# Optimization experiments

Hardware: AMD Instinct MI355X
Metric: run time of the kernel (lower is better)

Reference implementation:

```python
import jax, jax.numpy as jnp
import numpy as np

N, D_IN, D_H, D_ATT, N_CLUSTERS, N_CLASSES = 20000, 1024, 512, 256, 10, 4


def setup_inputs() -> dict:
    key = jax.random.key(0)
    ks = jax.random.split(key, 20)
    s = 0.02
    inp = {
        "x_path": jax.random.normal(ks[0], (N, D_IN), dtype=jnp.float32),
        "cluster_id": jax.random.randint(ks[1], (N,), 0, N_CLUSTERS, dtype=jnp.int64 if jax.config.jax_enable_x64 else jnp.int32),
        # per-cluster expert MLPs (phi_i): 1024->512->512
        "W1": jax.random.normal(ks[2], (N_CLUSTERS, D_IN, D_H), dtype=jnp.float32) * s,
        "b1": jnp.zeros((N_CLUSTERS, D_H), dtype=jnp.float32),
        "W2": jax.random.normal(ks[3], (N_CLUSTERS, D_H, D_H), dtype=jnp.float32) * s,
        "b2": jnp.zeros((N_CLUSTERS, D_H), dtype=jnp.float32),
        # attention_net: fc (512->512) then gated attention (L=512, D=256, 1)
        "Wfc": jax.random.normal(ks[4], (D_H, D_H), dtype=jnp.float32) * s,
        "bfc": jnp.zeros((D_H,), dtype=jnp.float32),
        "Wa": jax.random.normal(ks[5], (D_H, D_ATT), dtype=jnp.float32) * s,
        "ba": jnp.zeros((D_ATT,), dtype=jnp.float32),
        "Wb": jax.random.normal(ks[6], (D_H, D_ATT), dtype=jnp.float32) * s,
        "bb": jnp.zeros((D_ATT,), dtype=jnp.float32),
        "Wc": jax.random.normal(ks[7], (D_ATT, 1), dtype=jnp.float32) * s,
        "bc": jnp.zeros((1,), dtype=jnp.float32),
        # rho: 512->256
        "Wrho": jax.random.normal(ks[8], (D_H, D_ATT), dtype=jnp.float32) * s,
        "brho": jnp.zeros((D_ATT,), dtype=jnp.float32),
        # classifier: 256->4
        "Wcls": jax.random.normal(ks[9], (D_ATT, N_CLASSES), dtype=jnp.float32) * s,
        "bcls": jnp.zeros((N_CLASSES,), dtype=jnp.float32),
    }
    return inp


def reference(x_path, cluster_id, W1, b1, W2, b2, Wfc, bfc, Wa, ba, Wb, bb, Wc, bc, Wrho, brho, Wcls, bcls):
    C = W1.shape[0]
    # dispatch mask [N, C]; per-cluster counts
    onehot = jax.nn.one_hot(cluster_id, C, dtype=x_path.dtype)
    counts = jnp.maximum(onehot.sum(axis=0), 1.0)  # [C]
    # per-cluster expert MLP + masked mean-pool (AdaptiveAvgPool1d(1) over instances)
    pooled = []
    for i in range(C):  # small static loop over experts
        h = jax.nn.relu(x_path @ W1[i] + b1[i])      # [N, 512]
        h = jax.nn.relu(h @ W2[i] + b2[i])           # [N, 512]
        pooled.append((onehot[:, i] @ h) / counts[i])  # masked mean -> [512]
    h_cluster = jnp.stack(pooled, axis=0)            # [C, 512]
    # attention_net: fc then gated attention
    h = jax.nn.relu(h_cluster @ Wfc + bfc)           # [C, 512]
    a = jnp.tanh(h @ Wa + ba)                        # [C, 256]
    b = jax.nn.sigmoid(h @ Wb + bb)                  # [C, 256]
    A = ((a * b) @ Wc + bc).T                        # [1, C]
    A = jax.nn.softmax(A, axis=1)
    h_path = A @ h                                   # [1, 512]
    h_path = jax.nn.relu(h_path @ Wrho + brho).squeeze()  # [256]
    logits = (h_path @ Wcls + bcls)[None, :]         # [1, 4]
    Y_hat = jnp.argmax(logits, axis=1, keepdims=True)
    hazards = jax.nn.sigmoid(logits)
    S = jnp.cumprod(1.0 - hazards, axis=1)
    return hazards, S, Y_hat
```

## Files before the change

### kernel.cpp

```cpp
#include <hip/hip_runtime.h>
#include <hip/hip_bf16.h>
#include <math.h>


#define C_NUM 10
#define D_IN 1024
#define D_H 512
#define D_ATT 256
#define N_CLS 4
#define BM 128
#define BMG 64
#define BN 128
#define BKS 64

typedef __attribute__((ext_vector_type(8))) short short8v;
typedef __attribute__((ext_vector_type(4))) short short4v;
typedef __attribute__((ext_vector_type(4))) float f32x4;

__device__ __forceinline__ short f2bf(float f) {
    __hip_bfloat16 h = __float2bfloat16(f);
    return *reinterpret_cast<short*>(&h);
}

__device__ __forceinline__ void gload_lds16(const void* g, void* l) {
    __builtin_amdgcn_global_load_lds((const __attribute__((address_space(1))) unsigned int*)g,
                                     (__attribute__((address_space(3))) unsigned int*)l,
                                     16, 0, 0);
}

__device__ __forceinline__ int xcd_swizzle(int orig, int nwg) {
    int q = nwg >> 3, r = nwg & 7;
    int xcd = orig & 7, base = orig >> 3;
    return (xcd < r ? xcd * (q + 1) : r * (q + 1) + (xcd - r) * q) + base;
}

__global__ __launch_bounds__(256) void k_hist(const int* __restrict__ cid, int* counts, int n) {
    __shared__ int lc[C_NUM];
    int tid = threadIdx.x;
    if (tid < C_NUM) lc[tid] = 0;
    __syncthreads();
    int i = blockIdx.x * 256 + tid;
    if (i < n) atomicAdd(&lc[cid[i]], 1);
    __syncthreads();
    if (tid < C_NUM && lc[tid] > 0) atomicAdd(&counts[tid], lc[tid]);
}

__global__ __launch_bounds__(256) void k_scatter(const int* __restrict__ cid, int* cursor,
                                                 const int* __restrict__ counts,
                                                 int* bucket, int n) {
    __shared__ int lc[C_NUM];
    __shared__ int basev[C_NUM];
    __shared__ int loff[C_NUM + 1];
    int tid = threadIdx.x;
    if (tid < C_NUM) lc[tid] = 0;
    if (tid == 0) {
        int off = 0;
        for (int c2 = 0; c2 < C_NUM; ++c2) {
            loff[c2] = off;
            off += ((counts[c2] + BM - 1) / BM) * BM;
        }
        loff[C_NUM] = off;
    }
    __syncthreads();
    int i = blockIdx.x * 256 + tid;
    int c = 0, lpos = 0;
    bool valid = (i < n);
    if (valid) { c = cid[i]; lpos = atomicAdd(&lc[c], 1); }
    __syncthreads();
    if (tid < C_NUM) basev[tid] = (lc[tid] > 0) ? atomicAdd(&cursor[tid], lc[tid]) : 0;
    __syncthreads();
    if (valid) bucket[loff[c] + basev[c] + lpos] = i;
    if (blockIdx.x == 0) {
        for (int c2 = 0; c2 < C_NUM; ++c2)
            for (int p = loff[c2] + counts[c2] + tid; p < loff[c2 + 1]; p += 256)
                bucket[p] = -1;
    }
}

__global__ __launch_bounds__(256) void k_transpose2(
    const float* __restrict__ W1, short* __restrict__ Wt1,
    const float* __restrict__ W2, short* __restrict__ Wt2)
{
    __shared__ float t[64][65];
    int bid = blockIdx.x;
    const float* src; short* dst; int K, N, k0, n0;
    if (bid < C_NUM * 128) {
        int cc = bid >> 7, r = bid & 127;
        k0 = (r & 15) * 64; n0 = (r >> 4) * 64;
        src = W1 + (size_t)cc * D_IN * D_H; dst = Wt1 + (size_t)cc * D_H * D_IN;
        K = D_IN; N = D_H;
    } else {
        int idx = bid - C_NUM * 128;
        int cc = idx >> 6, r = idx & 63;
        k0 = (r & 7) * 64; n0 = (r >> 3) * 64;
        src = W2 + (size_t)cc * D_H * D_H; dst = Wt2 + (size_t)cc * D_H * D_H;
        K = D_H; N = D_H;
    }
    int tid = threadIdx.x;
    int tk = tid >> 4, tn4 = (tid & 15) * 4;
#pragma unroll
    for (int it = 0; it < 4; ++it) {
        int k = tk + it * 16;
        f32x4 v = *(const f32x4*)&src[(size_t)(k0 + k) * N + n0 + tn4];
        t[k][tn4 + 0] = v[0]; t[k][tn4 + 1] = v[1];
        t[k][tn4 + 2] = v[2]; t[k][tn4 + 3] = v[3];
    }
    __syncthreads();
    int wn = tid >> 2, kq = (tid & 3) * 16;
#pragma unroll
    for (int q = 0; q < 4; ++q) {
        int k = kq + q * 4;
        short4v o;
#pragma unroll
        for (int e = 0; e < 4; ++e) o[e] = f2bf(t[k + e][wn]);
        *(short4v*)&dst[(size_t)(n0 + wn) * K + k0 + k] = o;
    }
}

__global__ __launch_bounds__(256) void k_gemm1x64(
    const float* __restrict__ x, const short* __restrict__ Wt, const float* __restrict__ b1,
    const int* __restrict__ bucket, const int* __restrict__ counts, short* __restrict__ h1)
{
    __shared__ float Asf[BMG * BKS];
    __shared__ short Bs[BN * BKS];
    __shared__ int ridx[BMG];
    __shared__ int saoff[C_NUM + 1];

    int tid = threadIdx.x;
    if (tid == 0) {
        int off = 0;
        for (int c2 = 0; c2 < C_NUM; ++c2) {
            saoff[c2] = off;
            off += ((counts[c2] + BM - 1) / BM) * BM;
        }
        saoff[C_NUM] = off;
    }
    __syncthreads();

    int wg = xcd_swizzle(blockIdx.x, gridDim.x);
    int rowStart = (wg >> 2) * BMG;
    if (rowStart >= saoff[C_NUM]) return;
    int c = 0;
    while (c < C_NUM - 1 && rowStart >= saoff[c + 1]) ++c;
    int colStart = (wg & 3) * BN;

    int lane = tid & 63;
    int wid = tid >> 6;
    int wm = wid >> 1, wn = wid & 1;

    if (tid < BMG) ridx[tid] = bucket[rowStart + tid];
    __syncthreads();

    const float* aq[4];
#pragma unroll
    for (int q = 0; q < 4; ++q) {
        int row = q * 16 + wid * 4 + (lane >> 4);
        int rr = ridx[row];
        int srcslot = (lane & 15) ^ (row & 15);
        aq[q] = x + (size_t)(rr < 0 ? 0 : rr) * D_IN + srcslot * 4;
    }
    int l8 = lane >> 3;
    int sslot = (lane & 7) ^ l8;
    const short* bbase = Wt + ((size_t)c * D_H + colStart + l8) * D_IN + sslot * 8;

    f32x4 acc[2][4];
#pragma unroll
    for (int i = 0; i < 2; ++i)
#pragma unroll
        for (int j = 0; j < 4; ++j)
            acc[i][j] = f32x4{0.f, 0.f, 0.f, 0.f};

    for (int k0 = 0; k0 < D_IN; k0 += BKS) {
#pragma unroll
        for (int q = 0; q < 4; ++q) {
            int rb = (q * 4 + wid) * 8;
            gload_lds16(bbase + (size_t)rb * D_IN + k0, &Bs[rb * BKS]);
        }
#pragma unroll
        for (int q = 0; q < 4; ++q)
            gload_lds16(aq[q] + k0, &Asf[(q * 16 + wid * 4) * BKS]);
        __syncthreads();
#pragma unroll
        for (int kk = 0; kk < 2; ++kk) {
            short8v af[2], bfr[4];
#pragma unroll
            for (int i = 0; i < 2; ++i) {
                int row = wm * 32 + i * 16 + (lane & 15);
                int s8 = kk * 4 + (lane >> 4);
                int p0 = (2 * s8) ^ (row & 15);
                int p1 = (2 * s8 + 1) ^ (row & 15);
                f32x4 lo = *(const f32x4*)&Asf[row * BKS + p0 * 4];
                f32x4 hi = *(const f32x4*)&Asf[row * BKS + p1 * 4];
                short8v v;
#pragma unroll
                for (int e = 0; e < 4; ++e) { v[e] = f2bf(lo[e]); v[4 + e] = f2bf(hi[e]); }
                af[i] = v;
            }
#pragma unroll
            for (int j = 0; j < 4; ++j) {
                int nn = wn * 64 + j * 16 + (lane & 15);
                int slot = (kk * 4 + (lane >> 4)) ^ (nn & 7);
                bfr[j] = *(const short8v*)&Bs[nn * BKS + slot * 8];
            }
#pragma unroll
            for (int i = 0; i < 2; ++i)
#pragma unroll
                for (int j = 0; j < 4; ++j)
                    acc[i][j] = __builtin_amdgcn_mfma_f32_16x16x32_bf16(af[i], bfr[j], acc[i][j], 0, 0, 0);
        }
        __syncthreads();
    }

    const float* bias = b1 + c * D_H;
    float bj[4];
#pragma unroll
    for (int j = 0; j < 4; ++j) bj[j] = bias[colStart + wn * 64 + j * 16 + (lane & 15)];
#pragma unroll
    for (int i = 0; i < 2; ++i) {
#pragma unroll
        for (int r = 0; r < 4; ++r) {
            int rowl = wm * 32 + i * 16 + (lane >> 4) * 4 + r;
            bool valid = (ridx[rowl] >= 0);
            size_t gro = (size_t)(rowStart + rowl) * D_H + colStart + wn * 64 + (lane & 15);
#pragma unroll
            for (int j = 0; j < 4; ++j) {
                float v = valid ? fmaxf(acc[i][j][r] + bj[j], 0.f) : 0.f;
                h1[gro + j * 16] = f2bf(v);
            }
        }
    }
}

__global__ __launch_bounds__(256) void k_gemm2g64(
    const short* __restrict__ h1, const short* __restrict__ Wt, const float* __restrict__ b2,
    const int* __restrict__ bucket, const int* __restrict__ counts, float* __restrict__ pooled)
{
    __shared__ short As[BMG * BKS];
    __shared__ short Bs[BN * BKS];
    __shared__ int ridx[BMG];
    __shared__ int saoff[C_NUM + 1];

    int tid = threadIdx.x;
    if (tid == 0) {
        int off = 0;
        for (int c2 = 0; c2 < C_NUM; ++c2) {
            saoff[c2] = off;
            off += ((counts[c2] + BM - 1) / BM) * BM;
        }
        saoff[C_NUM] = off;
    }
    __syncthreads();

    int wg = xcd_swizzle(blockIdx.x, gridDim.x);
    int rowStart = (wg >> 2) * BMG;
    if (rowStart >= saoff[C_NUM]) return;
    int c = 0;
    while (c < C_NUM - 1 && rowStart >= saoff[c + 1]) ++c;
    int colStart = (wg & 3) * BN;

    int lane = tid & 63;
    int wid = tid >> 6;
    int wm = wid >> 1, wn = wid & 1;

    if (tid < BMG) ridx[tid] = bucket[rowStart + tid];

    int l8 = lane >> 3;
    int sslot = (lane & 7) ^ l8;
    const short* abase = h1 + (size_t)(rowStart + l8) * D_H + sslot * 8;
    const short* bbase = Wt + ((size_t)c * D_H + colStart + l8) * D_H + sslot * 8;

    f32x4 acc[2][4];
#pragma unroll
    for (int i = 0; i < 2; ++i)
#pragma unroll
        for (int j = 0; j < 4; ++j)
            acc[i][j] = f32x4{0.f, 0.f, 0.f, 0.f};

    for (int k0 = 0; k0 < D_H; k0 += BKS) {
#pragma unroll
        for (int q = 0; q < 2; ++q) {
            int rb = (q * 4 + wid) * 8;
            gload_lds16(abase + (size_t)rb * D_H + k0, &As[rb * BKS]);
        }
#pragma unroll
        for (int q = 0; q < 4; ++q) {
            int rb = (q * 4 + wid) * 8;
            gload_lds16(bbase + (size_t)rb * D_H + k0, &Bs[rb * BKS]);
        }
        __syncthreads();
#pragma unroll
        for (int kk = 0; kk < 2; ++kk) {
            short8v af[2], bfr[4];
#pragma unroll
            for (int i = 0; i < 2; ++i) {
                int row = wm * 32 + i * 16 + (lane & 15);
                int slot = (kk * 4 + (lane >> 4)) ^ (row & 7);
                af[i] = *(const short8v*)&As[row * BKS + slot * 8];
            }
#pragma unroll
            for (int j = 0; j < 4; ++j) {
                int nn = wn * 64 + j * 16 + (lane & 15);
                int slot = (kk * 4 + (lane >> 4)) ^ (nn & 7);
                bfr[j] = *(const short8v*)&Bs[nn * BKS + slot * 8];
            }
#pragma unroll
            for (int i = 0; i < 2; ++i)
#pragma unroll
                for (int j = 0; j < 4; ++j)
                    acc[i][j] = __builtin_amdgcn_mfma_f32_16x16x32_bf16(af[i], bfr[j], acc[i][j], 0, 0, 0);
        }
        __syncthreads();
    }

    const float* bias = b2 + c * D_H;
    float bj[4];
#pragma unroll
    for (int j = 0; j < 4; ++j) bj[j] = bias[colStart + wn * 64 + j * 16 + (lane & 15)];
    float csum[4] = {0.f, 0.f, 0.f, 0.f};
#pragma unroll
    for (int i = 0; i < 2; ++i) {
#pragma unroll
        for (int r = 0; r < 4; ++r) {
            int rowl = wm * 32 + i * 16 + (lane >> 4) * 4 + r;
            float m = (ridx[rowl] >= 0) ? 1.f : 0.f;
#pragma unroll
            for (int j = 0; j < 4; ++j)
                csum[j] += m * fmaxf(acc[i][j][r] + bj[j], 0.f);
        }
    }
#pragma unroll
    for (int j = 0; j < 4; ++j) {
        float s = csum[j];
        s += __shfl_xor(s, 16, 64);
        s += __shfl_xor(s, 32, 64);
        if ((lane >> 4) == 0)
            atomicAdd(&pooled[c * D_H + colStart + wn * 64 + j * 16 + lane], s);
    }
}

__global__ __launch_bounds__(256) void k_tA(
    const float* __restrict__ pooled, const int* __restrict__ counts,
    const float* __restrict__ Wfc, const float* __restrict__ bfc,
    float* __restrict__ hfc)
{
    __shared__ float hcs[C_NUM][D_H];
    __shared__ float red[4][64][C_NUM];
    int tid = threadIdx.x;
    for (int idx = tid; idx < C_NUM * D_H; idx += 256) {
        int cc = idx >> 9;
        hcs[cc][idx & (D_H - 1)] = pooled[idx] / fmaxf((float)counts[cc], 1.f);
    }
    __syncthreads();
    int col = blockIdx.x * 64 + (tid & 63);
    int kq = tid >> 6, k0 = kq * 128;
    float acc[C_NUM] = {};
    for (int k = 0; k < 128; ++k) {
        float wv = Wfc[(size_t)(k0 + k) * D_H + col];
#pragma unroll
        for (int cc = 0; cc < C_NUM; ++cc) acc[cc] += hcs[cc][k0 + k] * wv;
    }
#pragma unroll
    for (int cc = 0; cc < C_NUM; ++cc) red[kq][tid & 63][cc] = acc[cc];
    __syncthreads();
    if (kq == 0) {
        float bv = bfc[col];
#pragma unroll
        for (int cc = 0; cc < C_NUM; ++cc) {
            float s = red[0][tid][cc] + red[1][tid][cc] + red[2][tid][cc] + red[3][tid][cc];
            hfc[cc * D_H + col] = fmaxf(s + bv, 0.f);
        }
    }
}

__global__ __launch_bounds__(256) void k_tB(
    const float* __restrict__ hfc,
    const float* __restrict__ Wa, const float* __restrict__ ba,
    const float* __restrict__ Wb, const float* __restrict__ bb,
    const float* __restrict__ Wc,
    float* __restrict__ scores)
{
    __shared__ float hfs[C_NUM][D_H];
    __shared__ float red[4][64][C_NUM][2];
    int tid = threadIdx.x;
    for (int idx = tid; idx < C_NUM * D_H; idx += 256) {
        hfs[idx >> 9][idx & (D_H - 1)] = hfc[idx];
    }
    __syncthreads();
    int ad = blockIdx.x * 64 + (tid & 63);
    int kq = tid >> 6, k0 = kq * 128;
    float sa[C_NUM] = {}, sb[C_NUM] = {};
    for (int k = 0; k < 128; ++k) {
        float wav = Wa[(size_t)(k0 + k) * D_ATT + ad];
        float wbv = Wb[(size_t)(k0 + k) * D_ATT + ad];
#pragma unroll
        for (int cc = 0; cc < C_NUM; ++cc) {
            float h = hfs[cc][k0 + k];
            sa[cc] += h * wav;
            sb[cc] += h * wbv;
        }
    }
#pragma unroll
    for (int cc = 0; cc < C_NUM; ++cc) {
        red[kq][tid & 63][cc][0] = sa[cc];
        red[kq][tid & 63][cc][1] = sb[cc];
    }
    __syncthreads();
    if (kq == 0) {
        float bav = ba[ad], bbv = bb[ad], wcv = Wc[ad];
#pragma unroll
        for (int cc = 0; cc < C_NUM; ++cc) {
            float sat = red[0][tid][cc][0] + red[1][tid][cc][0] + red[2][tid][cc][0] + red[3][tid][cc][0];
            float sbt = red[0][tid][cc][1] + red[1][tid][cc][1] + red[2][tid][cc][1] + red[3][tid][cc][1];
            float v = tanhf(sat + bav) * (1.f / (1.f + expf(-(sbt + bbv)))) * wcv;
            v += __shfl_xor(v, 1, 64); v += __shfl_xor(v, 2, 64); v += __shfl_xor(v, 4, 64);
            v += __shfl_xor(v, 8, 64); v += __shfl_xor(v, 16, 64); v += __shfl_xor(v, 32, 64);
            if (tid == 0) atomicAdd(&scores[cc], v);
        }
    }
}

__global__ __launch_bounds__(256) void k_tCDE(
    const float* __restrict__ scores, const float* __restrict__ bc,
    const float* __restrict__ hfc, const float* __restrict__ Wrho,
    float* __restrict__ hr_raw, int* __restrict__ done,
    const float* __restrict__ brho,
    const float* __restrict__ Wcls, const float* __restrict__ bcls,
    float* __restrict__ out)
{
    __shared__ float hps[32];
    __shared__ int amLast;
    int tid = threadIdx.x;
    int k0 = blockIdx.x * 32;
    if (tid < 32) {
        float sc2[C_NUM];
        float mx = -1e30f;
#pragma unroll
        for (int cc = 0; cc < C_NUM; ++cc) { sc2[cc] = scores[cc] + bc[0]; mx = fmaxf(mx, sc2[cc]); }
        float sum = 0.f;
#pragma unroll
        for (int cc = 0; cc < C_NUM; ++cc) { sc2[cc] = expf(sc2[cc] - mx); sum += sc2[cc]; }
        float s = 0.f;
#pragma unroll
        for (int cc = 0; cc < C_NUM; ++cc) s += (sc2[cc] / sum) * hfc[cc * D_H + k0 + tid];
        hps[tid] = s;
    }
    __syncthreads();
    float acc = 0.f;
#pragma unroll 8
    for (int k = 0; k < 32; ++k)
        acc += hps[k] * Wrho[(size_t)(k0 + k) * D_ATT + tid];
    atomicAdd(&hr_raw[tid], acc);

    __threadfence();
    if (tid == 0) amLast = (atomicAdd(done, 1) == (int)gridDim.x - 1);
    __syncthreads();
    if (!amLast) return;

    __shared__ float cpart[4][N_CLS];
    int lane = tid & 63, w = tid >> 6;
    float hraw = atomicAdd(&hr_raw[tid], 0.f);
    float h = fmaxf(hraw + brho[tid], 0.f);
    f32x4 wv = *(const f32x4*)&Wcls[tid * N_CLS];
    float v[N_CLS];
#pragma unroll
    for (int l = 0; l < N_CLS; ++l) {
        v[l] = h * wv[l];
        v[l] += __shfl_xor(v[l], 1, 64); v[l] += __shfl_xor(v[l], 2, 64);
        v[l] += __shfl_xor(v[l], 4, 64); v[l] += __shfl_xor(v[l], 8, 64);
        v[l] += __shfl_xor(v[l], 16, 64); v[l] += __shfl_xor(v[l], 32, 64);
    }
    if (lane == 0) {
#pragma unroll
        for (int l = 0; l < N_CLS; ++l) cpart[w][l] = v[l];
    }
    __syncthreads();
    if (tid == 0) {
        float lg[N_CLS];
#pragma unroll
        for (int l = 0; l < N_CLS; ++l)
            lg[l] = cpart[0][l] + cpart[1][l] + cpart[2][l] + cpart[3][l] + bcls[l];
        int best = 0;
#pragma unroll
        for (int l = 1; l < N_CLS; ++l) if (lg[l] > lg[best]) best = l;
        float Sv = 1.f;
#pragma unroll
        for (int l = 0; l < N_CLS; ++l) {
            float hz = 1.f / (1.f + expf(-lg[l]));
            out[l] = hz;
            Sv *= (1.f - hz);
            out[4 + l] = Sv;
        }
        out[8] = (float)best;
    }
}

extern "C" void kernel_launch(void* const* d_in, const int* in_sizes, int n_in,
                              void* d_out, int out_size, void* d_ws, size_t ws_size,
                              hipStream_t stream)
{
    const float* x    = (const float*)d_in[0];
    const int*   cid  = (const int*)d_in[1];
    const float* W1   = (const float*)d_in[2];
    const float* b1   = (const float*)d_in[3];
    const float* W2   = (const float*)d_in[4];
    const float* b2   = (const float*)d_in[5];
    const float* Wfc  = (const float*)d_in[6];
    const float* bfc  = (const float*)d_in[7];
    const float* Wa   = (const float*)d_in[8];
    const float* ba   = (const float*)d_in[9];
    const float* Wb   = (const float*)d_in[10];
    const float* bb   = (const float*)d_in[11];
    const float* Wc   = (const float*)d_in[12];
    const float* bc   = (const float*)d_in[13];
    const float* Wrho = (const float*)d_in[14];
    const float* brho = (const float*)d_in[15];
    const float* Wcls = (const float*)d_in[16];
    const float* bcls = (const float*)d_in[17];
    float* out = (float*)d_out;

    int n = in_sizes[0] / D_IN;
    int rowTiles = (n + BM - 1) / BM + C_NUM;
    int npadMax = rowTiles * BM;
    int rowTiles64 = rowTiles * 2;

    char* w = (char*)d_ws;
    int* counts   = (int*)w;
    int* cursor   = counts + 16;
    float* scores = (float*)(counts + 32);
    int* done     = (int*)(scores + 16);
    float* hr_raw = (float*)(done + 16);
    float* pooled = hr_raw + 256;
    size_t zero_bytes = (size_t)(16 + 16 + 16 + 16 + 256 + 5120) * 4;
    float* hfc  = pooled + 5120;
    int* bucket = (int*)(hfc + 5120);
    short* Wt1 = (short*)(bucket + npadMax);
    short* Wt2 = Wt1 + (size_t)C_NUM * D_H * D_IN;
    short* h1  = Wt2 + (size_t)C_NUM * D_H * D_H;

    hipMemsetAsync(w, 0, zero_bytes, stream);

    int nb = (n + 255) / 256;
    k_hist<<<nb, 256, 0, stream>>>(cid, counts, n);
    k_scatter<<<nb, 256, 0, stream>>>(cid, cursor, counts, bucket, n);

    k_transpose2<<<C_NUM * 128 + C_NUM * 64, 256, 0, stream>>>(W1, Wt1, W2, Wt2);

    k_gemm1x64<<<rowTiles64 * 4, 256, 0, stream>>>(x, Wt1, b1, bucket, counts, h1);
    k_gemm2g64<<<rowTiles64 * 4, 256, 0, stream>>>(h1, Wt2, b2, bucket, counts, pooled);

    k_tA<<<8, 256, 0, stream>>>(pooled, counts, Wfc, bfc, hfc);
    k_tB<<<4, 256, 0, stream>>>(hfc, Wa, ba, Wb, bb, Wc, scores);
    k_tCDE<<<16, 256, 0, stream>>>(scores, bc, hfc, Wrho, hr_raw, done,
                                   brho, Wcls, bcls, out);
}
```

Before: 126.3 us.

## Double-buffer LDS tiles in both expert GEMMs and drop shared-memory prologue

```diff
diff --git a/kernel.cpp b/kernel.cpp
--- a/kernel.cpp
+++ b/kernel.cpp
@@ -12,6 +12,8 @@
 #define BMG 64
 #define BN 128
 #define BKS 64
+#define NT1 (D_IN / BKS)
+#define NT2 (D_H / BKS)
 
 typedef __attribute__((ext_vector_type(8))) short short8v;
 typedef __attribute__((ext_vector_type(4))) short short4v;
@@ -32,6 +34,17 @@
     int q = nwg >> 3, r = nwg & 7;
     int xcd = orig & 7, base = orig >> 3;
     return (xcd < r ? xcd * (q + 1) : r * (q + 1) + (xcd - r) * q) + base;
+}
+
+__device__ __forceinline__ int cluster_of(const int* counts, int rowStart, int* totalOut) {
+    int acco = 0, c = 0;
+#pragma unroll
+    for (int c2 = 0; c2 < C_NUM; ++c2) {
+        if (rowStart >= acco) c = c2;
+        acco += ((counts[c2] + BM - 1) / BM) * BM;
+    }
+    *totalOut = acco;
+    return c;
 }
 
 __global__ __launch_bounds__(256) void k_hist(const int* __restrict__ cid, int* counts, int n) {
@@ -117,45 +130,31 @@
     }
 }
 
-__global__ __launch_bounds__(256) void k_gemm1x64(
+__global__ __launch_bounds__(256) void k_gemm1d(
     const float* __restrict__ x, const short* __restrict__ Wt, const float* __restrict__ b1,
     const int* __restrict__ bucket, const int* __restrict__ counts, short* __restrict__ h1)
 {
-    __shared__ float Asf[BMG * BKS];
-    __shared__ short Bs[BN * BKS];
-    __shared__ int ridx[BMG];
-    __shared__ int saoff[C_NUM + 1];
-
-    int tid = threadIdx.x;
-    if (tid == 0) {
-        int off = 0;
-        for (int c2 = 0; c2 < C_NUM; ++c2) {
-            saoff[c2] = off;
-            off += ((counts[c2] + BM - 1) / BM) * BM;
-        }
-        saoff[C_NUM] = off;
-    }
-    __syncthreads();
-
+    __shared__ float Asf[2][BMG * BKS];
+    __shared__ short Bs[2][BN * BKS];
+
+    int tid = threadIdx.x;
     int wg = xcd_swizzle(blockIdx.x, gridDim.x);
     int rowStart = (wg >> 2) * BMG;
-    if (rowStart >= saoff[C_NUM]) return;
-    int c = 0;
-    while (c < C_NUM - 1 && rowStart >= saoff[c + 1]) ++c;
     int colStart = (wg & 3) * BN;
+
+    int total;
+    int c = cluster_of(counts, rowStart, &total);
+    if (rowStart >= total) return;
 
     int lane = tid & 63;
     int wid = tid >> 6;
     int wm = wid >> 1, wn = wid & 1;
 
-    if (tid < BMG) ridx[tid] = bucket[rowStart + tid];
-    __syncthreads();
-
     const float* aq[4];
 #pragma unroll
     for (int q = 0; q < 4; ++q) {
         int row = q * 16 + wid * 4 + (lane >> 4);
-        int rr = ridx[row];
+        int rr = bucket[rowStart + row];
         int srcslot = (lane & 15) ^ (row & 15);
         aq[q] = x + (size_t)(rr < 0 ? 0 : rr) * D_IN + srcslot * 4;
     }
@@ -170,16 +169,17 @@
         for (int j = 0; j < 4; ++j)
             acc[i][j] = f32x4{0.f, 0.f, 0.f, 0.f};
 
-    for (int k0 = 0; k0 < D_IN; k0 += BKS) {
+    auto STAGE = [&](int b, int k0) {
 #pragma unroll
         for (int q = 0; q < 4; ++q) {
             int rb = (q * 4 + wid) * 8;
-            gload_lds16(bbase + (size_t)rb * D_IN + k0, &Bs[rb * BKS]);
+            gload_lds16(bbase + (size_t)rb * D_IN + k0, &Bs[b][rb * BKS]);
         }
 #pragma unroll
         for (int q = 0; q < 4; ++q)
-            gload_lds16(aq[q] + k0, &Asf[(q * 16 + wid * 4) * BKS]);
-        __syncthreads();
+            gload_lds16(aq[q] + k0, &Asf[b][(q * 16 + wid * 4) * BKS]);
+    };
+    auto COMPUTE = [&](int b) {
 #pragma unroll
         for (int kk = 0; kk < 2; ++kk) {
             short8v af[2], bfr[4];
@@ -189,8 +189,8 @@
                 int s8 = kk * 4 + (lane >> 4);
                 int p0 = (2 * s8) ^ (row & 15);
                 int p1 = (2 * s8 + 1) ^ (row & 15);
-                f32x4 lo = *(const f32x4*)&Asf[row * BKS + p0 * 4];
-                f32x4 hi = *(const f32x4*)&Asf[row * BKS + p1 * 4];
+                f32x4 lo = *(const f32x4*)&Asf[b][row * BKS + p0 * 4];
+                f32x4 hi = *(const f32x4*)&Asf[b][row * BKS + p1 * 4];
                 short8v v;
 #pragma unroll
                 for (int e = 0; e < 4; ++e) { v[e] = f2bf(lo[e]); v[4 + e] = f2bf(hi[e]); }
@@ -200,7 +200,7 @@
             for (int j = 0; j < 4; ++j) {
                 int nn = wn * 64 + j * 16 + (lane & 15);
                 int slot = (kk * 4 + (lane >> 4)) ^ (nn & 7);
-                bfr[j] = *(const short8v*)&Bs[nn * BKS + slot * 8];
+                bfr[j] = *(const short8v*)&Bs[b][nn * BKS + slot * 8];
             }
 #pragma unroll
             for (int i = 0; i < 2; ++i)
@@ -208,8 +208,18 @@
                 for (int j = 0; j < 4; ++j)
                     acc[i][j] = __builtin_amdgcn_mfma_f32_16x16x32_bf16(af[i], bfr[j], acc[i][j], 0, 0, 0);
         }
+    };
+
+    STAGE(0, 0);
+    __syncthreads();
+    int cur = 0;
+    for (int t = 0; t < NT1 - 1; ++t) {
+        STAGE(cur ^ 1, (t + 1) * BKS);
+        COMPUTE(cur);
         __syncthreads();
-    }
+        cur ^= 1;
+    }
+    COMPUTE(cur);
 
     const float* bias = b1 + c * D_H;
     float bj[4];
@@ -220,7 +230,7 @@
 #pragma unroll
         for (int r = 0; r < 4; ++r) {
             int rowl = wm * 32 + i * 16 + (lane >> 4) * 4 + r;
-            bool valid = (ridx[rowl] >= 0);
+            bool valid = (bucket[rowStart + rowl] >= 0);
             size_t gro = (size_t)(rowStart + rowl) * D_H + colStart + wn * 64 + (lane & 15);
 #pragma unroll
             for (int j = 0; j < 4; ++j) {
@@ -231,38 +241,25 @@
     }
 }
 
-__global__ __launch_bounds__(256) void k_gemm2g64(
+__global__ __launch_bounds__(256) void k_gemm2d(
     const short* __restrict__ h1, const short* __restrict__ Wt, const float* __restrict__ b2,
     const int* __restrict__ bucket, const int* __restrict__ counts, float* __restrict__ pooled)
 {
-    __shared__ short As[BMG * BKS];
-    __shared__ short Bs[BN * BKS];
-    __shared__ int ridx[BMG];
-    __shared__ int saoff[C_NUM + 1];
-
-    int tid = threadIdx.x;
-    if (tid == 0) {
-        int off = 0;
-        for (int c2 = 0; c2 < C_NUM; ++c2) {
-            saoff[c2] = off;
-            off += ((counts[c2] + BM - 1) / BM) * BM;
-        }
-        saoff[C_NUM] = off;
-    }
-    __syncthreads();
-
+    __shared__ short As[2][BMG * BKS];
+    __shared__ short Bs[2][BN * BKS];
+
+    int tid = threadIdx.x;
     int wg = xcd_swizzle(blockIdx.x, gridDim.x);
     int rowStart = (wg >> 2) * BMG;
-    if (rowStart >= saoff[C_NUM]) return;
-    int c = 0;
-    while (c < C_NUM - 1 && rowStart >= saoff[c + 1]) ++c;
     int colStart = (wg & 3) * BN;
+
+    int total;
+    int c = cluster_of(counts, rowStart, &total);
+    if (rowStart >= total) return;
 
     int lane = tid & 63;
     int wid = tid >> 6;
     int wm = wid >> 1, wn = wid & 1;
-
-    if (tid < BMG) ridx[tid] = bucket[rowStart + tid];
 
     int l8 = lane >> 3;
     int sslot = (lane & 7) ^ l8;
@@ -276,18 +273,19 @@
         for (int j = 0; j < 4; ++j)
             acc[i][j] = f32x4{0.f, 0.f, 0.f, 0.f};
 
-    for (int k0 = 0; k0 < D_H; k0 += BKS) {
+    auto STAGE = [&](int b, int k0) {
 #pragma unroll
         for (int q = 0; q < 2; ++q) {
             int rb = (q * 4 + wid) * 8;
-            gload_lds16(abase + (size_t)rb * D_H + k0, &As[rb * BKS]);
+            gload_lds16(abase + (size_t)rb * D_H + k0, &As[b][rb * BKS]);
         }
 #pragma unroll
         for (int q = 0; q < 4; ++q) {
             int rb = (q * 4 + wid) * 8;
-            gload_lds16(bbase + (size_t)rb * D_H + k0, &Bs[rb * BKS]);
-        }
-        __syncthreads();
+            gload_lds16(bbase + (size_t)rb * D_H + k0, &Bs[b][rb * BKS]);
+        }
+    };
+    auto COMPUTE = [&](int b) {
 #pragma unroll
         for (int kk = 0; kk < 2; ++kk) {
             short8v af[2], bfr[4];
@@ -295,13 +293,13 @@
             for (int i = 0; i < 2; ++i) {
                 int row = wm * 32 + i * 16 + (lane & 15);
                 int slot = (kk * 4 + (lane >> 4)) ^ (row & 7);
-                af[i] = *(const short8v*)&As[row * BKS + slot * 8];
+                af[i] = *(const short8v*)&As[b][row * BKS + slot * 8];
             }
 #pragma unroll
             for (int j = 0; j < 4; ++j) {
                 int nn = wn * 64 + j * 16 + (lane & 15);
                 int slot = (kk * 4 + (lane >> 4)) ^ (nn & 7);
-                bfr[j] = *(const short8v*)&Bs[nn * BKS + slot * 8];
+                bfr[j] = *(const short8v*)&Bs[b][nn * BKS + slot * 8];
             }
 #pragma unroll
             for (int i = 0; i < 2; ++i)
@@ -309,8 +307,18 @@
                 for (int j = 0; j < 4; ++j)
                     acc[i][j] = __builtin_amdgcn_mfma_f32_16x16x32_bf16(af[i], bfr[j], acc[i][j], 0, 0, 0);
         }
+    };
+
+    STAGE(0, 0);
+    __syncthreads();
+    int cur = 0;
+    for (int t = 0; t < NT2 - 1; ++t) {
+        STAGE(cur ^ 1, (t + 1) * BKS);
+        COMPUTE(cur);
         __syncthreads();
-    }
+        cur ^= 1;
+    }
+    COMPUTE(cur);
 
     const float* bias = b2 + c * D_H;
     float bj[4];
@@ -322,7 +330,7 @@
 #pragma unroll
         for (int r = 0; r < 4; ++r) {
             int rowl = wm * 32 + i * 16 + (lane >> 4) * 4 + r;
-            float m = (ridx[rowl] >= 0) ? 1.f : 0.f;
+            float m = (bucket[rowStart + rowl] >= 0) ? 1.f : 0.f;
 #pragma unroll
             for (int j = 0; j < 4; ++j)
                 csum[j] += m * fmaxf(acc[i][j][r] + bj[j], 0.f);
@@ -545,8 +553,8 @@
 
     k_transpose2<<<C_NUM * 128 + C_NUM * 64, 256, 0, stream>>>(W1, Wt1, W2, Wt2);
 
-    k_gemm1x64<<<rowTiles64 * 4, 256, 0, stream>>>(x, Wt1, b1, bucket, counts, h1);
-    k_gemm2g64<<<rowTiles64 * 4, 256, 0, stream>>>(h1, Wt2, b2, bucket, counts, pooled);
+    k_gemm1d<<<rowTiles64 * 4, 256, 0, stream>>>(x, Wt1, b1, bucket, counts, h1);
+    k_gemm2d<<<rowTiles64 * 4, 256, 0, stream>>>(h1, Wt2, b2, bucket, counts, pooled);
 
     k_tA<<<8, 256, 0, stream>>>(pooled, counts, Wfc, bfc, hfc);
     k_tB<<<4, 256, 0, stream>>>(hfc, Wa, ba, Wb, bb, Wc, scores);
```

Measured after the change: 139.7 us. 10.7% more time.
